# Performance work log

Hardware: AMD Instinct MI355X
Metric: run time of the kernel (lower is better)

## Reference

```python
import jax, jax.numpy as jnp
import numpy as np

B, R, S, T, F = 16, 4, 4, 14, 2048  # batch, rx ants, streams, ofdm symbols, subcarriers


def setup_inputs() -> dict:
    key = jax.random.key(0)
    ks = jax.random.split(key, 5)
    y_re = jax.random.normal(ks[0], (B, R, T, F), jnp.float32)
    y_im = jax.random.normal(ks[1], (B, R, T, F), jnp.float32)
    h_re = jax.random.normal(ks[2], (B, R, S, T, F), jnp.float32)
    h_im = jax.random.normal(ks[3], (B, R, S, T, F), jnp.float32)
    mask = jax.random.randint(ks[4], (T, F), 0, 2, jnp.int32)  # MU_MIMO_RG_populated
    noise_var = jnp.array([0.1], jnp.float32)
    return {"y_re": y_re, "y_im": y_im, "h_re": h_re, "h_im": h_im,
            "mask": mask, "noise_var": noise_var}


def _sic_lmmse(y, h, no):
    # y: [B,T,F,R] complex, h: [B,T,F,R,S] complex, no: scalar noise variance
    eyeS = jnp.eye(S, dtype=jnp.complex64)
    y_res = y
    xs, ns = [], []
    for k in range(S):  # fixed detection order over the 4 streams
        m = (jnp.arange(S) >= k).astype(jnp.complex64)  # remaining (undetected) streams
        Hm = h * m  # zero out already-cancelled stream columns
        gram0 = jnp.einsum('...rs,...rt->...st', jnp.conj(Hm), Hm)  # [.,S,S] Hm^H Hm
        A = gram0 + no * eyeS                                        # LMMSE matrix
        Ainv = jnp.linalg.inv(A)                                     # batched 4x4 inverse
        z = jnp.einsum('...rs,...r->...s', jnp.conj(Hm), y_res)     # Hm^H y_res
        xz = jnp.einsum('...st,...t->...s', Ainv, z)                 # unbiased-unscaled estimate
        d = jnp.einsum('...t,...t->...', Ainv[..., k, :], gram0[..., :, k])  # (Ainv gram0)_kk
        xk = xz[..., k] / d                                          # bias-corrected LMMSE estimate
        ne = jnp.real((1.0 - d) / d)                                 # effective post-eq noise var
        y_res = y_res - h[..., :, k] * xk[..., None]                 # soft interference cancellation
        xs.append(xk)
        ns.append(ne)
    x_hat = jnp.stack(xs, -1)   # [B,T,F,S]
    no_eff = jnp.stack(ns, -1)  # [B,T,F,S]
    return x_hat, no_eff


def reference(y_re, y_im, h_re, h_im, mask, noise_var):
    y = jax.lax.complex(y_re, y_im)             # [B,R,T,F]
    h = jax.lax.complex(h_re, h_im)             # [B,R,S,T,F]
    y = jnp.transpose(y, (0, 2, 3, 1))          # [B,T,F,R]
    h = jnp.transpose(h, (0, 3, 4, 1, 2))       # [B,T,F,R,S]
    no = noise_var[0]
    x_hat, no_eff = _sic_lmmse(y, h, no)
    m = mask.astype(jnp.float32)[None, :, :, None]  # populated-RE mask [1,T,F,1]
    x_hat = x_hat * m
    no_eff = no_eff * m
    x_hat = jnp.transpose(x_hat, (0, 3, 1, 2))   # [B,S,T,F]
    no_eff = jnp.transpose(no_eff, (0, 3, 1, 2))
    x_ri = jnp.stack([jnp.real(x_hat), jnp.imag(x_hat)], 0)  # [2,B,S,T,F] real view
    return x_ri, no_eff
```

## Files before the change

kernel.cpp:

```cpp
#include <hip/hip_runtime.h>
#include <math.h>

#define B_ 16
#define R_ 4
#define S_ 4
#define T_ 14
#define F_ 2048

struct cplx { float re, im; };

__device__ __forceinline__ cplx cmul(cplx a, cplx b) {
    return {a.re*b.re - a.im*b.im, a.re*b.im + a.im*b.re};
}
__device__ __forceinline__ cplx cmulc(cplx a, cplx b) {
    return {a.re*b.re + a.im*b.im, a.re*b.im - a.im*b.re};
}
__device__ __forceinline__ cplx cadd(cplx a, cplx b) { return {a.re+b.re, a.im+b.im}; }
__device__ __forceinline__ cplx csub(cplx a, cplx b) { return {a.re-b.re, a.im-b.im}; }
__device__ __forceinline__ cplx cscale(cplx a, float s) { return {a.re*s, a.im*s}; }
__device__ __forceinline__ cplx conjc(cplx a) { return {a.re, -a.im}; }

__global__ __launch_bounds__(256) void sic_lmmse_kernel(
    const float* __restrict__ y_re, const float* __restrict__ y_im,
    const float* __restrict__ h_re, const float* __restrict__ h_im,
    const int* __restrict__ mask, const float* __restrict__ nv,
    float* __restrict__ out)
{
    constexpr int TF  = T_ * F_;
    constexpr int N   = B_ * TF;
    constexpr int BST = B_ * S_ * TF;

    int idx = blockIdx.x * 256 + threadIdx.x;
    if (idx >= N) return;

    int f  = idx % F_;
    int bt = idx / F_;
    int t  = bt % T_;
    int b  = bt / T_;

    float no = nv[0];
    float m  = (float)mask[t * F_ + f];

    cplx g[4][4];
    cplx z[4];
    #pragma unroll
    for (int i = 0; i < 4; i++) {
        z[i] = {0.f, 0.f};
        #pragma unroll
        for (int j = 0; j <= i; j++) g[i][j] = {0.f, 0.f};
    }

    #pragma unroll
    for (int r = 0; r < 4; r++) {
        int ybase = ((b * R_ + r) * T_ + t) * F_ + f;
        cplx yr = { y_re[ybase], y_im[ybase] };
        cplx hr[4];
        #pragma unroll
        for (int s = 0; s < 4; s++) {
            int hbase = (((b * R_ + r) * S_ + s) * T_ + t) * F_ + f;
            hr[s] = { h_re[hbase], h_im[hbase] };
        }
        #pragma unroll
        for (int s = 0; s < 4; s++) {
            z[s] = cadd(z[s], cmulc(hr[s], yr));
            #pragma unroll
            for (int u = 0; u <= s; u++)
                g[s][u] = cadd(g[s][u], cmulc(hr[s], hr[u]));
        }
    }

    cplx Lm[4][4];
    float dinv[4];
    #pragma unroll
    for (int i = 0; i < 4; i++) {
        #pragma unroll
        for (int j = 0; j < i; j++) {
            cplx s = g[i][j];
            #pragma unroll
            for (int p = 0; p < j; p++)
                s = csub(s, cmul(Lm[i][p], conjc(Lm[j][p])));
            Lm[i][j] = cscale(s, dinv[j]);
        }
        float dd = g[i][i].re + no;
        #pragma unroll
        for (int p = 0; p < i; p++)
            dd -= Lm[i][p].re * Lm[i][p].re + Lm[i][p].im * Lm[i][p].im;
        float ld = sqrtf(dd);
        dinv[i] = 1.0f / ld;
        Lm[i][i] = { ld, 0.f };
    }

    cplx M[4][4];
    #pragma unroll
    for (int i = 0; i < 4; i++) {
        #pragma unroll
        for (int j = 0; j < i; j++) {
            cplx s = {0.f, 0.f};
            #pragma unroll
            for (int p = j; p < i; p++)
                s = cadd(s, cmul(Lm[i][p], M[p][j]));
            M[i][j] = cscale(s, -dinv[i]);
        }
        M[i][i] = { dinv[i], 0.f };
    }

    cplx W[4][4];
    #pragma unroll
    for (int i = 0; i < 4; i++) {
        #pragma unroll
        for (int j = 0; j <= i; j++) {
            cplx s = {0.f, 0.f};
            #pragma unroll
            for (int p = i; p < 4; p++)
                s = cadd(s, cmul(conjc(M[p][i]), M[p][j]));
            W[i][j] = s;
        }
    }

    cplx zc[4];
    #pragma unroll
    for (int j = 0; j < 4; j++) zc[j] = z[j];

    #pragma unroll
    for (int k = 0; k < 4; k++) {
        const int n = 4 - k;
        float e = W[0][0].re;
        cplx xz = cscale(zc[0], e);
        #pragma unroll
        for (int j = 1; j < 4; j++) {
            if (j < n) xz = cadd(xz, cmul(conjc(W[j][0]), zc[j]));
        }
        float d    = 1.0f - no * e;
        float drcp = 1.0f / d;
        cplx  xk   = cscale(xz, drcp);
        float ne   = no * e * drcp;

        int obase = ((b * S_ + k) * T_ + t) * F_ + f;
        out[obase]            = xk.re * m;
        out[BST + obase]      = xk.im * m;
        out[2 * BST + obase]  = ne * m;

        if (k < 3) {
            float einv = 1.0f / e;
            #pragma unroll
            for (int j = 1; j < 4; j++) {
                if (j < n) zc[j - 1] = csub(zc[j], cmul(g[k + j][k], xk));
            }
            cplx W2[3][3];
            #pragma unroll
            for (int i = 1; i < 4; i++) {
                #pragma unroll
                for (int j = 1; j <= i; j++) {
                    if (i < n)
                        W2[i - 1][j - 1] =
                            csub(W[i][j], cscale(cmul(W[i][0], conjc(W[j][0])), einv));
                }
            }
            #pragma unroll
            for (int i = 0; i < 3; i++) {
                #pragma unroll
                for (int j = 0; j <= i; j++) {
                    if (i < n - 1) W[i][j] = W2[i][j];
                }
            }
        }
    }
}

extern "C" void kernel_launch(void* const* d_in, const int* in_sizes, int n_in,
                              void* d_out, int out_size, void* d_ws, size_t ws_size,
                              hipStream_t stream) {
    const float* y_re = (const float*)d_in[0];
    const float* y_im = (const float*)d_in[1];
    const float* h_re = (const float*)d_in[2];
    const float* h_im = (const float*)d_in[3];
    const int*   mask = (const int*)  d_in[4];
    const float* nv   = (const float*)d_in[5];
    float* out = (float*)d_out;

    constexpr int N = B_ * T_ * F_;
    int threads = 256;
    int blocks  = (N + threads - 1) / threads;
    hipLaunchKernelGGL(sic_lmmse_kernel, dim3(blocks), dim3(threads), 0, stream,
                       y_re, y_im, h_re, h_im, mask, nv, out);
}
```

Before: 112.7 us.

## Process two subcarriers per thread with float2 vectors and fast rcp/rsqrt

```diff
diff --git a/kernel.cpp b/kernel.cpp
--- a/kernel.cpp
+++ b/kernel.cpp
@@ -1,13 +1,19 @@
 #include <hip/hip_runtime.h>
-#include <math.h>
 
 #define B_ 16
 #define R_ 4
 #define S_ 4
 #define T_ 14
 #define F_ 2048
+constexpr int P_ = F_ / 2;
 
-struct cplx { float re, im; };
+typedef float vf __attribute__((ext_vector_type(2)));
+
+struct cplx { vf re, im; };
+
+__device__ __forceinline__ vf vsp(float s){ vf r; r.x = s; r.y = s; return r; }
+__device__ __forceinline__ vf vrcp(vf x){ vf r; r.x = __builtin_amdgcn_rcpf(x.x); r.y = __builtin_amdgcn_rcpf(x.y); return r; }
+__device__ __forceinline__ vf vrsq(vf x){ vf r; r.x = __builtin_amdgcn_rsqf(x.x); r.y = __builtin_amdgcn_rsqf(x.y); return r; }
 
 __device__ __forceinline__ cplx cmul(cplx a, cplx b) {
     return {a.re*b.re - a.im*b.im, a.re*b.im + a.im*b.re};
@@ -15,49 +21,55 @@
 __device__ __forceinline__ cplx cmulc(cplx a, cplx b) {
     return {a.re*b.re + a.im*b.im, a.re*b.im - a.im*b.re};
 }
-__device__ __forceinline__ cplx cadd(cplx a, cplx b) { return {a.re+b.re, a.im+b.im}; }
-__device__ __forceinline__ cplx csub(cplx a, cplx b) { return {a.re-b.re, a.im-b.im}; }
-__device__ __forceinline__ cplx cscale(cplx a, float s) { return {a.re*s, a.im*s}; }
-__device__ __forceinline__ cplx conjc(cplx a) { return {a.re, -a.im}; }
+__device__ __forceinline__ cplx cadd(cplx a, cplx b){ return {a.re+b.re, a.im+b.im}; }
+__device__ __forceinline__ cplx csub(cplx a, cplx b){ return {a.re-b.re, a.im-b.im}; }
+__device__ __forceinline__ cplx cscale(cplx a, vf s){ return {a.re*s, a.im*s}; }
+__device__ __forceinline__ cplx conjc(cplx a){ return {a.re, -a.im}; }
 
 __global__ __launch_bounds__(256) void sic_lmmse_kernel(
-    const float* __restrict__ y_re, const float* __restrict__ y_im,
-    const float* __restrict__ h_re, const float* __restrict__ h_im,
+    const float* __restrict__ y_re_, const float* __restrict__ y_im_,
+    const float* __restrict__ h_re_, const float* __restrict__ h_im_,
     const int* __restrict__ mask, const float* __restrict__ nv,
-    float* __restrict__ out)
+    float* __restrict__ out_)
 {
-    constexpr int TF  = T_ * F_;
-    constexpr int N   = B_ * TF;
-    constexpr int BST = B_ * S_ * TF;
+    constexpr int N    = B_ * T_ * P_;
+    constexpr int BSTP = B_ * S_ * T_ * P_;
 
     int idx = blockIdx.x * 256 + threadIdx.x;
-    if (idx >= N) return;
-
-    int f  = idx % F_;
-    int bt = idx / F_;
+    int fv = idx % P_;
+    int bt = idx / P_;
     int t  = bt % T_;
     int b  = bt / T_;
 
-    float no = nv[0];
-    float m  = (float)mask[t * F_ + f];
+    const vf* y_re = (const vf*)y_re_;
+    const vf* y_im = (const vf*)y_im_;
+    const vf* h_re = (const vf*)h_re_;
+    const vf* h_im = (const vf*)h_im_;
+    vf*       out  = (vf*)out_;
+
+    float no  = nv[0];
+    vf    vno = vsp(no);
+
+    int2 mi = ((const int2*)mask)[t * P_ + fv];
+    vf m; m.x = (float)mi.x; m.y = (float)mi.y;
 
     cplx g[4][4];
     cplx z[4];
     #pragma unroll
     for (int i = 0; i < 4; i++) {
-        z[i] = {0.f, 0.f};
+        z[i] = { vsp(0.f), vsp(0.f) };
         #pragma unroll
-        for (int j = 0; j <= i; j++) g[i][j] = {0.f, 0.f};
+        for (int j = 0; j <= i; j++) g[i][j] = { vsp(0.f), vsp(0.f) };
     }
 
     #pragma unroll
     for (int r = 0; r < 4; r++) {
-        int ybase = ((b * R_ + r) * T_ + t) * F_ + f;
+        int ybase = ((b * R_ + r) * T_ + t) * P_ + fv;
         cplx yr = { y_re[ybase], y_im[ybase] };
         cplx hr[4];
         #pragma unroll
         for (int s = 0; s < 4; s++) {
-            int hbase = (((b * R_ + r) * S_ + s) * T_ + t) * F_ + f;
+            int hbase = (((b * R_ + r) * S_ + s) * T_ + t) * P_ + fv;
             hr[s] = { h_re[hbase], h_im[hbase] };
         }
         #pragma unroll
@@ -70,7 +82,7 @@
     }
 
     cplx Lm[4][4];
-    float dinv[4];
+    vf dinv[4];
     #pragma unroll
     for (int i = 0; i < 4; i++) {
         #pragma unroll
@@ -81,13 +93,11 @@
                 s = csub(s, cmul(Lm[i][p], conjc(Lm[j][p])));
             Lm[i][j] = cscale(s, dinv[j]);
         }
-        float dd = g[i][i].re + no;
+        vf dd = g[i][i].re + vno;
         #pragma unroll
         for (int p = 0; p < i; p++)
-            dd -= Lm[i][p].re * Lm[i][p].re + Lm[i][p].im * Lm[i][p].im;
-        float ld = sqrtf(dd);
-        dinv[i] = 1.0f / ld;
-        Lm[i][i] = { ld, 0.f };
+            dd = dd - (Lm[i][p].re * Lm[i][p].re + Lm[i][p].im * Lm[i][p].im);
+        dinv[i] = vrsq(dd);
     }
 
     cplx M[4][4];
@@ -95,13 +105,13 @@
     for (int i = 0; i < 4; i++) {
         #pragma unroll
         for (int j = 0; j < i; j++) {
-            cplx s = {0.f, 0.f};
+            cplx s = { vsp(0.f), vsp(0.f) };
             #pragma unroll
             for (int p = j; p < i; p++)
                 s = cadd(s, cmul(Lm[i][p], M[p][j]));
             M[i][j] = cscale(s, -dinv[i]);
         }
-        M[i][i] = { dinv[i], 0.f };
+        M[i][i] = { dinv[i], vsp(0.f) };
     }
 
     cplx W[4][4];
@@ -109,7 +119,7 @@
     for (int i = 0; i < 4; i++) {
         #pragma unroll
         for (int j = 0; j <= i; j++) {
-            cplx s = {0.f, 0.f};
+            cplx s = { vsp(0.f), vsp(0.f) };
             #pragma unroll
             for (int p = i; p < 4; p++)
                 s = cadd(s, cmul(conjc(M[p][i]), M[p][j]));
@@ -124,24 +134,24 @@
     #pragma unroll
     for (int k = 0; k < 4; k++) {
         const int n = 4 - k;
-        float e = W[0][0].re;
+        vf e = W[0][0].re;
         cplx xz = cscale(zc[0], e);
         #pragma unroll
         for (int j = 1; j < 4; j++) {
             if (j < n) xz = cadd(xz, cmul(conjc(W[j][0]), zc[j]));
         }
-        float d    = 1.0f - no * e;
-        float drcp = 1.0f / d;
-        cplx  xk   = cscale(xz, drcp);
-        float ne   = no * e * drcp;
+        vf d    = vsp(1.0f) - vno * e;
+        vf drcp = vrcp(d);
+        cplx xk = cscale(xz, drcp);
+        vf ne   = vno * e * drcp;
 
-        int obase = ((b * S_ + k) * T_ + t) * F_ + f;
+        int obase = ((b * S_ + k) * T_ + t) * P_ + fv;
         out[obase]            = xk.re * m;
-        out[BST + obase]      = xk.im * m;
-        out[2 * BST + obase]  = ne * m;
+        out[BSTP + obase]     = xk.im * m;
+        out[2 * BSTP + obase] = ne * m;
 
         if (k < 3) {
-            float einv = 1.0f / e;
+            vf einv = vrcp(e);
             #pragma unroll
             for (int j = 1; j < 4; j++) {
                 if (j < n) zc[j - 1] = csub(zc[j], cmul(g[k + j][k], xk));
@@ -178,9 +188,9 @@
     const float* nv   = (const float*)d_in[5];
     float* out = (float*)d_out;
 
-    constexpr int N = B_ * T_ * F_;
+    constexpr int N = B_ * T_ * P_;
     int threads = 256;
-    int blocks  = (N + threads - 1) / threads;
+    int blocks  = N / threads;
     hipLaunchKernelGGL(sic_lmmse_kernel, dim3(blocks), dim3(threads), 0, stream,
                        y_re, y_im, h_re, h_im, mask, nv, out);
 }
```

Result: no change. 111.7 us (-0.9%).
